# Kernel optimization log

Hardware: AMD Instinct MI355X
Metric: run time of the kernel (lower is better)

## Reference

```python
import jax, jax.numpy as jnp
import numpy as np
import math

B, S, D = 2, 2048, 4096
NH, NKV = 32, 8
HD = D // NH            # 128
NREP = NH // NKV        # 4
KV = S                  # start_pos=0, kv_len = start_pos + seqlen


def setup_inputs() -> dict:
    key = jax.random.key(0)
    ks = jax.random.split(key, 9)
    x = jax.random.normal(ks[0], (B, S, D), dtype=jnp.float32)
    freqs_cis = jax.random.uniform(ks[1], (S, HD // 2), dtype=jnp.float32, minval=-1.0, maxval=1.0)
    # causal mask (additive), large negative above diagonal
    mask = jnp.triu(jnp.full((S, KV), -1e9, dtype=jnp.float32), k=1)
    sc = 0.02
    wq = jax.random.normal(ks[2], (NH * HD, D), dtype=jnp.float32) * sc
    wk = jax.random.normal(ks[3], (NKV * HD, D), dtype=jnp.float32) * sc
    wv = jax.random.normal(ks[4], (NKV * HD, D), dtype=jnp.float32) * sc
    wo = jax.random.normal(ks[5], (D, NH * HD), dtype=jnp.float32) * sc
    cache_k = jax.random.normal(ks[6], (B, KV, NKV, HD), dtype=jnp.float32)
    cache_v = jax.random.normal(ks[7], (B, KV, NKV, HD), dtype=jnp.float32)
    return {"x": x, "freqs_cis": freqs_cis, "mask": mask,
            "wq": wq, "wk": wk, "wv": wv, "wo": wo,
            "cache_k": cache_k, "cache_v": cache_v}


def reference(x, freqs_cis, mask, wq, wk, wv, wo, cache_k, cache_v):
    scale = 1.0 / math.sqrt(HD)
    # QKV projections (wk/wv outputs are dead in the original forward: the
    # cache is read but never written, so keys/values come from cache only).
    xq = (x @ wq.T).reshape(B, S, NH, HD)
    # "rotary" as written in the source: elementwise multiply by tiled freqs
    fc = jnp.tile(freqs_cis, (1, 2))[None, :, None, :]   # (1,S,1,HD)
    xq = xq * fc
    keys = cache_k    # (B,KV,NKV,HD)
    values = cache_v
    # GQA: avoid materializing repeat_kv; group query heads per kv head
    q = xq.reshape(B, S, NKV, NREP, HD)
    scores = jnp.einsum('bqgrh,bkgh->bgrqk', q, keys) * scale
    scores = scores + mask                                # (q,k) broadcasts
    probs = jax.nn.softmax(scores.astype(jnp.float32), axis=-1).astype(xq.dtype)
    out = jnp.einsum('bgrqk,bkgh->bqgrh', probs, values)  # (B,S,NKV,NREP,HD)
    out = out.reshape(B, S, NH * HD)
    return out @ wo.T
```

## Files before the change

kernel.cpp:

```cpp
#include <hip/hip_runtime.h>


typedef __attribute__((ext_vector_type(8))) __bf16 bf16x8;
typedef __attribute__((ext_vector_type(4))) float f32x4;

#define S_LEN 2048
#define DMODEL 4096
#define NKV 8
#define HD 128

__device__ __forceinline__ bf16x8 cvt8(const float* __restrict__ p) {
  float4 f0 = *(const float4*)p, f1 = *(const float4*)(p + 4);
  bf16x8 v;
  v[0] = (__bf16)f0.x; v[1] = (__bf16)f0.y; v[2] = (__bf16)f0.z; v[3] = (__bf16)f0.w;
  v[4] = (__bf16)f1.x; v[5] = (__bf16)f1.y; v[6] = (__bf16)f1.z; v[7] = (__bf16)f1.w;
  return v;
}

__device__ __forceinline__ bf16x8 cvt8r(float4 f0, float4 f1) {
  bf16x8 v;
  v[0] = (__bf16)f0.x; v[1] = (__bf16)f0.y; v[2] = (__bf16)f0.z; v[3] = (__bf16)f0.w;
  v[4] = (__bf16)f1.x; v[5] = (__bf16)f1.y; v[6] = (__bf16)f1.z; v[7] = (__bf16)f1.w;
  return v;
}

template <int A_BF16, int EPI>
__global__ __launch_bounds__(256) void gemm_bt(
    const void* __restrict__ Av, const float* __restrict__ Bw,
    void* __restrict__ Cv, const float* __restrict__ freqs) {
  __shared__ __attribute__((aligned(16))) __bf16 As[128 * 72];
  __shared__ __attribute__((aligned(16))) __bf16 Bs[128 * 72];
  const int t = threadIdx.x;
  const int wave = t >> 6, lane = t & 63;
  const int l15 = lane & 15, quad = lane >> 4;
  const int wm = wave >> 1, wn = wave & 1;
  const int m0 = blockIdx.y * 128, n0 = blockIdx.x * 128;
  f32x4 acc[4][4] = {};
  for (int k0 = 0; k0 < DMODEL; k0 += 64) {
#pragma unroll
    for (int i = 0; i < 4; ++i) {
      int c = i * 256 + t;
      int r = c >> 3, col8 = (c & 7) * 8;
      if (A_BF16) {
        *(float4*)&As[r * 72 + col8] =
            *(const float4*)&((const __bf16*)Av)[(size_t)(m0 + r) * DMODEL + k0 + col8];
      } else {
        *(bf16x8*)&As[r * 72 + col8] =
            cvt8(&((const float*)Av)[(size_t)(m0 + r) * DMODEL + k0 + col8]);
      }
      *(bf16x8*)&Bs[r * 72 + col8] =
          cvt8(&Bw[(size_t)(n0 + r) * DMODEL + k0 + col8]);
    }
    __syncthreads();
#pragma unroll
    for (int ks = 0; ks < 2; ++ks) {
      bf16x8 af[4], bfr[4];
#pragma unroll
      for (int i = 0; i < 4; ++i) {
        af[i]  = *(const bf16x8*)&As[(wm * 64 + i * 16 + l15) * 72 + ks * 32 + quad * 8];
        bfr[i] = *(const bf16x8*)&Bs[(wn * 64 + i * 16 + l15) * 72 + ks * 32 + quad * 8];
      }
#pragma unroll
      for (int mi = 0; mi < 4; ++mi)
#pragma unroll
        for (int ni = 0; ni < 4; ++ni)
          acc[mi][ni] = __builtin_amdgcn_mfma_f32_16x16x32_bf16(
              af[mi], bfr[ni], acc[mi][ni], 0, 0, 0);
    }
    __syncthreads();
  }
#pragma unroll
  for (int mi = 0; mi < 4; ++mi) {
    int rowb = m0 + wm * 64 + mi * 16 + quad * 4;
#pragma unroll
    for (int ni = 0; ni < 4; ++ni) {
      int col = n0 + wn * 64 + ni * 16 + l15;
#pragma unroll
      for (int r = 0; r < 4; ++r) {
        float v = acc[mi][ni][r];
        if (EPI == 1) {
          int s = (rowb + r) & (S_LEN - 1);
          v *= freqs[s * 64 + (col & 63)];
          ((__bf16*)Cv)[(size_t)(rowb + r) * DMODEL + col] = (__bf16)v;
        } else {
          ((float*)Cv)[(size_t)(rowb + r) * DMODEL + col] = v;
        }
      }
    }
  }
}

__global__ __launch_bounds__(256, 2) void attn_fwd(
    __bf16* __restrict__ QO, const float* __restrict__ K,
    const float* __restrict__ V) {
  __shared__ __attribute__((aligned(16))) __bf16 Ks[2][64 * 128];
  __shared__ __attribute__((aligned(16))) __bf16 Vs[2][128 * 72];
  __shared__ __attribute__((aligned(16))) __bf16 Ps[4][16 * 72];
  const int qt = blockIdx.x, h = blockIdx.y, b = blockIdx.z;
  const int g = h >> 2;
  const int t = threadIdx.x, wave = t >> 6, lane = t & 63;
  const int l15 = lane & 15, quad = lane >> 4;
  const int kx = l15 & 7;

  bf16x8 qf[2][4];
#pragma unroll
  for (int rb = 0; rb < 2; ++rb) {
    const __bf16* qb =
        QO + (size_t)(b * S_LEN + qt * 128 + rb * 64 + wave * 16 + l15) * DMODEL + h * HD;
#pragma unroll
    for (int kk = 0; kk < 4; ++kk) qf[rb][kk] = *(const bf16x8*)&qb[kk * 32 + quad * 8];
  }
  f32x4 of[2][8] = {};
  float m_r[2][4], l_r[2][4];
#pragma unroll
  for (int rb = 0; rb < 2; ++rb)
#pragma unroll
    for (int r = 0; r < 4; ++r) { m_r[rb][r] = -1e30f; l_r[rb][r] = 0.f; }

  const float* kbase = K + ((size_t)b * S_LEN * NKV + g) * HD;
  const float* vbase = V + ((size_t)b * S_LEN * NKV + g) * HD;
  const float scale = 0.08838834764831845f;
  const int KTMAX = 2 * qt + 1;

  float4 kre[8], vre[8];

  auto LOADT = [&](int kt) {
    const float* kr = kbase + (size_t)(kt * 64) * (NKV * HD);
    const float* vr = vbase + (size_t)(kt * 64) * (NKV * HD);
#pragma unroll
    for (int i = 0; i < 4; ++i) {
      int c = i * 256 + t, r = c >> 4, col8 = (c & 15) * 8;
      const float* kp = &kr[(size_t)r * (NKV * HD) + col8];
      const float* vp = &vr[(size_t)r * (NKV * HD) + col8];
      kre[2 * i]     = *(const float4*)kp;
      kre[2 * i + 1] = *(const float4*)(kp + 4);
      vre[2 * i]     = *(const float4*)vp;
      vre[2 * i + 1] = *(const float4*)(vp + 4);
    }
  };
  auto WRITET = [&](int d) {
#pragma unroll
    for (int i = 0; i < 4; ++i) {
      int c = i * 256 + t, r = c >> 4, col8 = (c & 15) * 8;
      *(bf16x8*)&Ks[d][r * 128 + (((col8 >> 3) ^ (r & 7)) << 3)] =
          cvt8r(kre[2 * i], kre[2 * i + 1]);
      bf16x8 vv = cvt8r(vre[2 * i], vre[2 * i + 1]);
      const int rblk = r >> 3, rin = r & 7;
#pragma unroll
      for (int j = 0; j < 8; ++j) {
        const int hd = col8 + j;
        const int blk = (rblk ^ (hd >> 4)) & 7;
        Vs[d][hd * 72 + blk * 8 + rin] = vv[j];
      }
    }
  };

  LOADT(0);
  WRITET(0);
  __syncthreads();
  int cur = 0;
  for (int kt = 0; kt <= KTMAX; ++kt) {
    if (kt < KTMAX) LOADT(kt + 1);
#pragma unroll
    for (int rb = 0; rb < 2; ++rb) {
      if (kt <= 2 * qt + rb) {
        f32x4 sf[4] = {};
#pragma unroll
        for (int kk = 0; kk < 4; ++kk)
#pragma unroll
          for (int ni = 0; ni < 4; ++ni) {
            const int kv = ni * 16 + l15;
            bf16x8 kf = *(const bf16x8*)&Ks[cur][kv * 128 + (((kk * 4 + quad) ^ kx) << 3)];
            sf[ni] = __builtin_amdgcn_mfma_f32_16x16x32_bf16(qf[rb][kk], kf, sf[ni], 0, 0, 0);
          }
        const int rowg = qt * 128 + rb * 64 + wave * 16 + quad * 4;
#pragma unroll
        for (int r = 0; r < 4; ++r) {
          float sv[4];
#pragma unroll
          for (int ni = 0; ni < 4; ++ni) {
            float v = sf[ni][r] * scale;
            int col = kt * 64 + ni * 16 + l15;
            if (col > rowg + r) v = -1e9f;
            sv[ni] = v;
          }
          float mx = fmaxf(fmaxf(sv[0], sv[1]), fmaxf(sv[2], sv[3]));
#pragma unroll
          for (int off = 1; off < 16; off <<= 1) mx = fmaxf(mx, __shfl_xor(mx, off, 64));
          float mn = fmaxf(m_r[rb][r], mx);
          float alpha = __expf(m_r[rb][r] - mn);
          float sum = 0.f;
#pragma unroll
          for (int ni = 0; ni < 4; ++ni) {
            float p = __expf(sv[ni] - mn);
            sum += p;
            sf[ni][r] = p;
          }
#pragma unroll
          for (int off = 1; off < 16; off <<= 1) sum += __shfl_xor(sum, off, 64);
          l_r[rb][r] = l_r[rb][r] * alpha + sum;
          m_r[rb][r] = mn;
#pragma unroll
          for (int nf = 0; nf < 8; ++nf) of[rb][nf][r] *= alpha;
        }
#pragma unroll
        for (int ni = 0; ni < 4; ++ni)
#pragma unroll
          for (int r = 0; r < 4; ++r)
            Ps[wave][(quad * 4 + r) * 72 + ni * 16 + l15] = (__bf16)sf[ni][r];
        asm volatile("s_waitcnt lgkmcnt(0)" ::: "memory");
#pragma unroll
        for (int kb = 0; kb < 2; ++kb) {
          bf16x8 pf = *(const bf16x8*)&Ps[wave][l15 * 72 + kb * 32 + quad * 8];
#pragma unroll
          for (int nf = 0; nf < 8; ++nf) {
            const int hd = nf * 16 + l15;
            const int blk = ((kb * 4 + quad) ^ (hd >> 4)) & 7;
            bf16x8 vf = *(const bf16x8*)&Vs[cur][hd * 72 + blk * 8];
            of[rb][nf] = __builtin_amdgcn_mfma_f32_16x16x32_bf16(pf, vf, of[rb][nf], 0, 0, 0);
          }
        }
      }
    }
    if (kt < KTMAX) WRITET(cur ^ 1);
    __syncthreads();
    cur ^= 1;
  }
#pragma unroll
  for (int rb = 0; rb < 2; ++rb)
#pragma unroll
    for (int r = 0; r < 4; ++r) {
      float inv = 1.0f / l_r[rb][r];
      size_t row = (size_t)(b * S_LEN + qt * 128 + rb * 64 + wave * 16 + quad * 4 + r);
#pragma unroll
      for (int nf = 0; nf < 8; ++nf)
        QO[row * DMODEL + h * HD + nf * 16 + l15] = (__bf16)(of[rb][nf][r] * inv);
    }
}

extern "C" void kernel_launch(void* const* d_in, const int* in_sizes, int n_in,
                              void* d_out, int out_size, void* d_ws, size_t ws_size,
                              hipStream_t stream) {
  const float* x     = (const float*)d_in[0];
  const float* freqs = (const float*)d_in[1];
  const float* wq = (const float*)d_in[3];
  const float* wo = (const float*)d_in[6];
  const float* ck = (const float*)d_in[7];
  const float* cv = (const float*)d_in[8];

  __bf16* q_ws = (__bf16*)d_ws;

  gemm_bt<0, 1><<<dim3(32, 32), 256, 0, stream>>>(x, wq, q_ws, freqs);
  attn_fwd<<<dim3(16, 32, 2), 256, 0, stream>>>(q_ws, ck, cv);
  gemm_bt<1, 0><<<dim3(32, 32), 256, 0, stream>>>(q_ws, wo, (float*)d_out, nullptr);
}
```

Before: 1.097 ms.

## Pre-convert inputs to bf16 and stream tiles into LDS with global_load_lds

Adds separate conversion kernels that turn x, wq, wo and the K/V caches into bf16 in workspace, when the workspace is large enough. New bf16 GEMM and attention paths then load tiles straight into LDS with global_load_lds and XOR swizzled addressing, so loads no longer go through registers. This halves the bytes read by the main kernels and removes in-loop conversion, at the cost of five extra conversion passes over roughly 224 MB of fp32 data each call. The GEMM loses its register-staged overlap because it syncs right after issuing the loads.

```diff
diff --git a/kernel.cpp b/kernel.cpp
--- a/kernel.cpp
+++ b/kernel.cpp
@@ -22,6 +22,84 @@
   v[0] = (__bf16)f0.x; v[1] = (__bf16)f0.y; v[2] = (__bf16)f0.z; v[3] = (__bf16)f0.w;
   v[4] = (__bf16)f1.x; v[5] = (__bf16)f1.y; v[6] = (__bf16)f1.z; v[7] = (__bf16)f1.w;
   return v;
+}
+
+__device__ __forceinline__ void gl_lds16(const __bf16* g, __bf16* l) {
+  __builtin_amdgcn_global_load_lds(
+      (const __attribute__((address_space(1))) void*)g,
+      (__attribute__((address_space(3))) void*)l, 16, 0, 0);
+}
+
+__global__ __launch_bounds__(256) void cvt_bf16(
+    const float* __restrict__ in, __bf16* __restrict__ out, int n8) {
+  int i = blockIdx.x * blockDim.x + threadIdx.x;
+  if (i < n8) *(bf16x8*)&out[(size_t)i * 8] = cvt8(&in[(size_t)i * 8]);
+}
+
+template <int EPI>
+__global__ __launch_bounds__(256) void gemm_bb(
+    const __bf16* __restrict__ A, const __bf16* __restrict__ B,
+    void* __restrict__ Cv, const float* __restrict__ freqs) {
+  __shared__ __attribute__((aligned(16))) __bf16 As[128 * 64];
+  __shared__ __attribute__((aligned(16))) __bf16 Bs[128 * 64];
+  const int t = threadIdx.x;
+  const int wave = t >> 6, lane = t & 63;
+  const int l15 = lane & 15, quad = lane >> 4;
+  const int wm = wave >> 1, wn = wave & 1;
+  const int m0 = blockIdx.y * 128, n0 = blockIdx.x * 128;
+  const int sl_chunk0 = wave;
+  const int sl_rowoff = lane >> 3;
+  const int sl_c8 = (lane & 7) ^ (lane >> 3);
+  f32x4 acc[4][4] = {};
+  for (int k0 = 0; k0 < DMODEL; k0 += 64) {
+#pragma unroll
+    for (int i = 0; i < 4; ++i) {
+      const int chunkid = i * 4 + sl_chunk0;
+      const int row = chunkid * 8 + sl_rowoff;
+      gl_lds16(&A[(size_t)(m0 + row) * DMODEL + k0 + sl_c8 * 8],
+               &As[chunkid * 512 + lane * 8]);
+      gl_lds16(&B[(size_t)(n0 + row) * DMODEL + k0 + sl_c8 * 8],
+               &Bs[chunkid * 512 + lane * 8]);
+    }
+    __syncthreads();
+#pragma unroll
+    for (int ks = 0; ks < 2; ++ks) {
+      bf16x8 af[4], bfr[4];
+#pragma unroll
+      for (int i = 0; i < 4; ++i) {
+        const int ar = wm * 64 + i * 16 + l15;
+        const int br = wn * 64 + i * 16 + l15;
+        af[i]  = *(const bf16x8*)&As[ar * 64 + (((ks * 4 + quad) ^ (ar & 7)) << 3)];
+        bfr[i] = *(const bf16x8*)&Bs[br * 64 + (((ks * 4 + quad) ^ (br & 7)) << 3)];
+      }
+#pragma unroll
+      for (int mi = 0; mi < 4; ++mi)
+#pragma unroll
+        for (int ni = 0; ni < 4; ++ni)
+          acc[mi][ni] = __builtin_amdgcn_mfma_f32_16x16x32_bf16(
+              af[mi], bfr[ni], acc[mi][ni], 0, 0, 0);
+    }
+    __syncthreads();
+  }
+#pragma unroll
+  for (int mi = 0; mi < 4; ++mi) {
+    int rowb = m0 + wm * 64 + mi * 16 + quad * 4;
+#pragma unroll
+    for (int ni = 0; ni < 4; ++ni) {
+      int col = n0 + wn * 64 + ni * 16 + l15;
+#pragma unroll
+      for (int r = 0; r < 4; ++r) {
+        float v = acc[mi][ni][r];
+        if (EPI == 1) {
+          int s = (rowb + r) & (S_LEN - 1);
+          v *= freqs[s * 64 + (col & 63)];
+          ((__bf16*)Cv)[(size_t)(rowb + r) * DMODEL + col] = (__bf16)v;
+        } else {
+          ((float*)Cv)[(size_t)(rowb + r) * DMODEL + col] = v;
+        }
+      }
+    }
+  }
 }
 
 template <int A_BF16, int EPI>
@@ -90,9 +168,10 @@
   }
 }
 
+template <int KVBF>
 __global__ __launch_bounds__(256, 2) void attn_fwd(
-    __bf16* __restrict__ QO, const float* __restrict__ K,
-    const float* __restrict__ V) {
+    __bf16* __restrict__ QO, const void* __restrict__ Kp,
+    const void* __restrict__ Vp) {
   __shared__ __attribute__((aligned(16))) __bf16 Ks[2][64 * 128];
   __shared__ __attribute__((aligned(16))) __bf16 Vs[2][128 * 72];
   __shared__ __attribute__((aligned(16))) __bf16 Ps[4][16 * 72];
@@ -117,16 +196,50 @@
 #pragma unroll
     for (int r = 0; r < 4; ++r) { m_r[rb][r] = -1e30f; l_r[rb][r] = 0.f; }
 
-  const float* kbase = K + ((size_t)b * S_LEN * NKV + g) * HD;
-  const float* vbase = V + ((size_t)b * S_LEN * NKV + g) * HD;
+  const float* kb32 = (const float*)Kp + ((size_t)b * S_LEN * NKV + g) * HD;
+  const float* vb32 = (const float*)Vp + ((size_t)b * S_LEN * NKV + g) * HD;
+  const __bf16* kb16 = (const __bf16*)Kp + ((size_t)b * S_LEN * NKV + g) * HD;
+  const __bf16* vb16 = (const __bf16*)Vp + ((size_t)b * S_LEN * NKV + g) * HD;
   const float scale = 0.08838834764831845f;
   const int KTMAX = 2 * qt + 1;
 
   float4 kre[8], vre[8];
-
-  auto LOADT = [&](int kt) {
-    const float* kr = kbase + (size_t)(kt * 64) * (NKV * HD);
-    const float* vr = vbase + (size_t)(kt * 64) * (NKV * HD);
+  bf16x8 vreb[4];
+
+  auto ISSUEK = [&](int kt, int d) {
+#pragma unroll
+    for (int i = 0; i < 4; ++i) {
+      const int chunkid = i * 4 + wave;
+      const int kv = chunkid * 4 + (lane >> 4);
+      const int hd8 = (lane & 15) ^ (kv & 7);
+      gl_lds16(&kb16[(size_t)(kt * 64 + kv) * (NKV * HD) + hd8 * 8],
+               &Ks[d][chunkid * 512 + lane * 8]);
+    }
+  };
+  auto LOADV16 = [&](int kt) {
+#pragma unroll
+    for (int i = 0; i < 4; ++i) {
+      int c = i * 256 + t, r = c >> 4, col8 = (c & 15) * 8;
+      vreb[i] = *(const bf16x8*)&vb16[(size_t)(kt * 64 + r) * (NKV * HD) + col8];
+    }
+  };
+  auto WRITEV16 = [&](int d) {
+#pragma unroll
+    for (int i = 0; i < 4; ++i) {
+      int c = i * 256 + t, r = c >> 4, col8 = (c & 15) * 8;
+      bf16x8 vv = vreb[i];
+      const int rblk = r >> 3, rin = r & 7;
+#pragma unroll
+      for (int j = 0; j < 8; ++j) {
+        const int hd = col8 + j;
+        const int blk = (rblk ^ (hd >> 4)) & 7;
+        Vs[d][hd * 72 + blk * 8 + rin] = vv[j];
+      }
+    }
+  };
+  auto LOADT32 = [&](int kt) {
+    const float* kr = kb32 + (size_t)(kt * 64) * (NKV * HD);
+    const float* vr = vb32 + (size_t)(kt * 64) * (NKV * HD);
 #pragma unroll
     for (int i = 0; i < 4; ++i) {
       int c = i * 256 + t, r = c >> 4, col8 = (c & 15) * 8;
@@ -138,7 +251,7 @@
       vre[2 * i + 1] = *(const float4*)(vp + 4);
     }
   };
-  auto WRITET = [&](int d) {
+  auto WRITET32 = [&](int d) {
 #pragma unroll
     for (int i = 0; i < 4; ++i) {
       int c = i * 256 + t, r = c >> 4, col8 = (c & 15) * 8;
@@ -155,12 +268,25 @@
     }
   };
 
-  LOADT(0);
-  WRITET(0);
+  if (KVBF) {
+    ISSUEK(0, 0);
+    LOADV16(0);
+    WRITEV16(0);
+  } else {
+    LOADT32(0);
+    WRITET32(0);
+  }
   __syncthreads();
   int cur = 0;
   for (int kt = 0; kt <= KTMAX; ++kt) {
-    if (kt < KTMAX) LOADT(kt + 1);
+    if (kt < KTMAX) {
+      if (KVBF) {
+        ISSUEK(kt + 1, cur ^ 1);
+        LOADV16(kt + 1);
+      } else {
+        LOADT32(kt + 1);
+      }
+    }
 #pragma unroll
     for (int rb = 0; rb < 2; ++rb) {
       if (kt <= 2 * qt + rb) {
@@ -222,7 +348,10 @@
         }
       }
     }
-    if (kt < KTMAX) WRITET(cur ^ 1);
+    if (kt < KTMAX) {
+      if (KVBF) WRITEV16(cur ^ 1);
+      else      WRITET32(cur ^ 1);
+    }
     __syncthreads();
     cur ^= 1;
   }
@@ -249,8 +378,28 @@
   const float* cv = (const float*)d_in[8];
 
   __bf16* q_ws = (__bf16*)d_ws;
-
-  gemm_bt<0, 1><<<dim3(32, 32), 256, 0, stream>>>(x, wq, q_ws, freqs);
-  attn_fwd<<<dim3(16, 32, 2), 256, 0, stream>>>(q_ws, ck, cv);
-  gemm_bt<1, 0><<<dim3(32, 32), 256, 0, stream>>>(q_ws, wo, (float*)d_out, nullptr);
-}
+  const size_t NE = (size_t)DMODEL * DMODEL;
+  const size_t NKVE = (size_t)2 * S_LEN * NKV * HD;
+  const size_t NEED = (NE * 4 + NKVE * 2) * sizeof(__bf16) + NE * sizeof(__bf16);
+
+  if (ws_size >= NEED) {
+    __bf16* x_bf  = q_ws + NE;
+    __bf16* wq_bf = q_ws + 2 * NE;
+    __bf16* wo_bf = q_ws + 3 * NE;
+    __bf16* k_bf  = q_ws + 4 * NE;
+    __bf16* v_bf  = k_bf + NKVE;
+    const int n8w = (int)(NE / 8), n8kv = (int)(NKVE / 8);
+    cvt_bf16<<<dim3(n8w / 256), 256, 0, stream>>>(x, x_bf, n8w);
+    cvt_bf16<<<dim3(n8w / 256), 256, 0, stream>>>(wq, wq_bf, n8w);
+    cvt_bf16<<<dim3(n8w / 256), 256, 0, stream>>>(wo, wo_bf, n8w);
+    cvt_bf16<<<dim3(n8kv / 256), 256, 0, stream>>>(ck, k_bf, n8kv);
+    cvt_bf16<<<dim3(n8kv / 256), 256, 0, stream>>>(cv, v_bf, n8kv);
+    gemm_bb<1><<<dim3(32, 32), 256, 0, stream>>>(x_bf, wq_bf, q_ws, freqs);
+    attn_fwd<1><<<dim3(16, 32, 2), 256, 0, stream>>>(q_ws, k_bf, v_bf);
+    gemm_bb<0><<<dim3(32, 32), 256, 0, stream>>>(q_ws, wo_bf, (float*)d_out, nullptr);
+  } else {
+    gemm_bt<0, 1><<<dim3(32, 32), 256, 0, stream>>>(x, wq, q_ws, freqs);
+    attn_fwd<0><<<dim3(16, 32, 2), 256, 0, stream>>>(q_ws, ck, cv);
+    gemm_bt<1, 0><<<dim3(32, 32), 256, 0, stream>>>(q_ws, wo, (float*)d_out, nullptr);
+  }
+}
```

Result: faster. 925.8 us (-15.6%).
